# Optimization experiments

Measured on AMD Instinct MI355X. Metric: run time of the kernel, lower is better.

Reference implementation:

```python
import jax, jax.numpy as jnp
import numpy as np

N_NODES = 50000
N_EDGES = 600000  # incidence entries; hyperedge ids also live in [0, N_NODES)
HID = 128


def _prelu(x, a):
    return jnp.where(x >= 0, x, a * x)


def _hypergraph_conv(x, W, b, node_idx, edge_idx, num_nodes, num_hedges):
    # PyG HypergraphConv (use_attention=False, heads=1):
    # out = D^{-1} H B^{-1} H^T (X Theta) + bias
    xw = x @ W  # [N, F]
    ones = jnp.ones(node_idx.shape[0], dtype=x.dtype)
    D = jax.ops.segment_sum(ones, node_idx, num_segments=num_nodes)   # node degree
    B = jax.ops.segment_sum(ones, edge_idx, num_segments=num_hedges)  # hyperedge degree
    Dinv = jnp.where(D > 0, 1.0 / D, 0.0)
    Binv = jnp.where(B > 0, 1.0 / B, 0.0)
    # node -> hyperedge aggregation, scaled by B^{-1}
    m = jax.ops.segment_sum(xw[node_idx], edge_idx, num_segments=num_hedges) * Binv[:, None]
    # hyperedge -> node aggregation, scaled by D^{-1}
    out = jax.ops.segment_sum(m[edge_idx], node_idx, num_segments=num_nodes) * Dinv[:, None]
    return out + b


def setup_inputs() -> dict:
    key = jax.random.key(0)
    k1, k2, k3, k4, k5 = jax.random.split(key, 5)
    x = jax.random.normal(k1, (N_NODES, HID), dtype=jnp.float32)
    hyper_edge_index = jax.random.randint(k2, (2, N_EDGES), 0, N_NODES, dtype=jnp.int64)
    # kaiming-normal-ish linear weights, zero biases (per init_weights)
    std = float(np.sqrt(2.0 / HID))
    W1 = jax.random.normal(k3, (HID, HID), dtype=jnp.float32) * std
    W2 = jax.random.normal(k4, (HID, HID), dtype=jnp.float32) * std
    b1 = jnp.zeros((HID,), dtype=jnp.float32)
    b2 = jnp.zeros((HID,), dtype=jnp.float32)
    prelu_a = jnp.full((1,), 0.25, dtype=jnp.float32)  # nn.PReLU default
    return {"x": x, "hyper_edge_index": hyper_edge_index,
            "W1": W1, "b1": b1, "W2": W2, "b2": b2, "prelu_a": prelu_a}


def reference(x, hyper_edge_index, W1, b1, W2, b2, prelu_a):
    node_idx = hyper_edge_index[0]
    edge_idx = hyper_edge_index[1]
    h = _hypergraph_conv(x, W1, b1, node_idx, edge_idx, N_NODES, N_NODES)
    h = _prelu(h, prelu_a)
    h = _hypergraph_conv(h, W2, b2, node_idx, edge_idx, N_NODES, N_NODES)
    h = h + x  # residual
    return _prelu(h, prelu_a)
```

## Files before the change

kernel.cpp:

```cpp
#include <hip/hip_runtime.h>

typedef unsigned short u16;
typedef unsigned int   u32;
typedef unsigned long long u64;

#define HID 128
#define KPB 256
#define NBMAX 512
#define IPB 2048
#define CAP 6144

typedef __bf16 bf16x8 __attribute__((ext_vector_type(8)));
typedef float  f32x4  __attribute__((ext_vector_type(4)));
typedef u32    u32x4  __attribute__((ext_vector_type(4)));

__device__ inline float u2f(u32 u){ union{u32 u;float f;} v; v.u=u; return v.f; }
__device__ inline u32   f2u(float f){ union{float f;u32 u;} v; v.f=f; return v.u; }
__device__ inline u32  f2bfu(float f){ u32 b=f2u(f); return ((b + 0x7FFFu + ((b>>16)&1u))>>16)&0xFFFFu; }
__device__ inline float blo(u32 u){ return u2f(u<<16); }
__device__ inline float bhi(u32 u){ return u2f(u & 0xFFFF0000u); }
__device__ inline u32  pk(float lo, float hi){ return (f2bfu(hi)<<16) | f2bfu(lo); }


__global__ __launch_bounds__(256) void k_hist_wfrag(const int* __restrict__ nidx, const int* __restrict__ eidx,
                                                    int* __restrict__ hist, int nE, int nN, int nb, int nhb,
                                                    const float* __restrict__ W1, const float* __restrict__ W2,
                                                    u16* __restrict__ W1f, u16* __restrict__ W2f){
    __shared__ int h[NBMAX];
    if ((int)blockIdx.x < nhb){
        for (int t=threadIdx.x; t<nb; t+=256) h[t]=0;
        __syncthreads();
        int base = blockIdx.x*IPB;
        for (int k=threadIdx.x; k<IPB; k+=256){
            int j = base+k;
            if (j < nE){
                atomicAdd(&h[nidx[j]>>8], 1);
                atomicAdd(&h[(nN+eidx[j])>>8], 1);
            }
        }
        __syncthreads();
        for (int t=threadIdx.x; t<nb; t+=256) if (h[t]) atomicAdd(&hist[t], h[t]);
    } else {
        int gid = ((int)blockIdx.x - nhb)*256 + threadIdx.x;
        const float* W = (gid < 16384) ? W1 : W2;
        u16* Wf = (gid < 16384) ? W1f : W2f;
        int id = gid & 16383;
        int i = id & 7, l = (id>>3)&63, j = (id>>9)&7, s = id>>12;
        Wf[id] = (u16)f2bfu(W[(s*32 + ((l>>4)<<3) + i)*HID + (j<<4) + (l&15)]);
    }
}

__global__ __launch_bounds__(256) void k_part_gemm(const int* __restrict__ nidx, const int* __restrict__ eidx,
                                                   const int* __restrict__ hist, int* __restrict__ bfill,
                                                   u64* __restrict__ pairs, int nE, int nN, int nb, int npb,
                                                   const float* __restrict__ A, const u16* __restrict__ Wf,
                                                   u16* __restrict__ C, int M){
    __shared__ int h[NBMAX], rsv[NBMAX], fl[NBMAX], bb[NBMAX], sd[256];
    int t = threadIdx.x;
    if ((int)blockIdx.x < npb){
        for (int i=t; i<nb; i+=256){ h[i]=0; fl[i]=0; }
        __syncthreads();
        int base = blockIdx.x*IPB;
        for (int k=t; k<IPB; k+=256){
            int j = base+k;
            if (j < nE){
                atomicAdd(&h[nidx[j]>>8], 1);
                atomicAdd(&h[(nN+eidx[j])>>8], 1);
            }
        }
        int c0 = (2*t   < nb) ? hist[2*t]   : 0;
        int c1 = (2*t+1 < nb) ? hist[2*t+1] : 0;
        int s = c0 + c1;
        sd[t] = s; __syncthreads();
        for (int o=1;o<256;o<<=1){ int u = (t>=o)? sd[t-o] : 0; __syncthreads(); sd[t]+=u; __syncthreads(); }
        int ex = sd[t] - s;
        if (2*t   < nb) bb[2*t]   = ex;
        if (2*t+1 < nb) bb[2*t+1] = ex + c0;
        __syncthreads();
        for (int i=t; i<nb; i+=256){ if (h[i]) rsv[i] = bb[i] + atomicAdd(&bfill[i], h[i]); }
        __syncthreads();
        for (int k=t; k<IPB; k+=256){
            int j = base+k;
            if (j < nE){
                int n = nidx[j], e = eidx[j];
                int b1 = n>>8;
                int p1 = rsv[b1] + atomicAdd(&fl[b1], 1);
                pairs[p1] = ((u64)(u32)n << 32) | (u32)e;
                int k2 = nN + e;
                int b2 = k2>>8;
                int p2 = rsv[b2] + atomicAdd(&fl[b2], 1);
                pairs[p2] = ((u64)(u32)k2 << 32) | (u32)n;
            }
        }
    } else {
        int wave = ((int)blockIdx.x - npb)*4 + (t>>6);
        int lane = t & 63;
        int rtiles = M >> 4;
        if (wave >= rtiles) return;
        int row0 = wave << 4;
        const float* Arow = A + (size_t)(row0 + (lane&15))*HID + ((lane>>4)<<3);
        const bf16x8* Wp = reinterpret_cast<const bf16x8*>(Wf) + lane;
        f32x4 acc[8];
        #pragma unroll
        for (int j=0;j<8;++j) acc[j] = (f32x4){0.f,0.f,0.f,0.f};
        #pragma unroll
        for (int s=0;s<4;++s){
            float4 f0 = *reinterpret_cast<const float4*>(Arow + s*32);
            float4 f1 = *reinterpret_cast<const float4*>(Arow + s*32 + 4);
            union { u16 h[8]; bf16x8 v; } au;
            au.h[0]=(u16)f2bfu(f0.x); au.h[1]=(u16)f2bfu(f0.y); au.h[2]=(u16)f2bfu(f0.z); au.h[3]=(u16)f2bfu(f0.w);
            au.h[4]=(u16)f2bfu(f1.x); au.h[5]=(u16)f2bfu(f1.y); au.h[6]=(u16)f2bfu(f1.z); au.h[7]=(u16)f2bfu(f1.w);
            #pragma unroll
            for (int j=0;j<8;++j){
                bf16x8 b = Wp[(s*8 + j)*64];
                acc[j] = __builtin_amdgcn_mfma_f32_16x16x32_bf16(au.v, b, acc[j], 0, 0, 0);
            }
        }
        int r0 = row0 + ((lane>>4)<<2);
        int c0 = lane & 15;
        #pragma unroll
        for (int j=0;j<8;++j){
            size_t sb = ((size_t)(j>>2)*M)*64 + ((j&3)<<4) + c0;
            #pragma unroll
            for (int r=0;r<4;++r){
                __builtin_nontemporal_store((u16)f2bfu(acc[j][r]), &C[sb + (size_t)(r0+r)*64]);
            }
        }
    }
}

__global__ __launch_bounds__(256) void k_bucket(const u64* __restrict__ pairs, const int* __restrict__ hist,
                                                int* __restrict__ csr, int* __restrict__ off,
                                                int nkeys, int nb, int total){
    __shared__ int cntS[KPB];
    __shared__ int fillS[KPB];
    __shared__ int bbS[NBMAX+1];
    __shared__ int sd[256];
    __shared__ int vals[CAP];
    int b = blockIdx.x;
    int t = threadIdx.x;
    if (b == 0 && t == 0) off[nkeys] = total;
    int c0 = (2*t   < nb) ? hist[2*t]   : 0;
    int c1 = (2*t+1 < nb) ? hist[2*t+1] : 0;
    int s = c0 + c1;
    sd[t] = s; __syncthreads();
    for (int o=1;o<256;o<<=1){ int u = (t>=o)? sd[t-o] : 0; __syncthreads(); sd[t]+=u; __syncthreads(); }
    int ex = sd[t] - s;
    if (2*t   <= nb) bbS[2*t]   = ex;
    if (2*t+1 <= nb) bbS[2*t+1] = ex + c0;
    __syncthreads();
    int base = bbS[b];
    int n = bbS[b+1] - base;
    int k0 = b * KPB;

    cntS[t] = 0;
    __syncthreads();
    for (int i=t; i<n; i+=256){
        u64 p = pairs[base+i];
        atomicAdd(&cntS[(int)(p>>32) - k0], 1);
    }
    __syncthreads();
    int c = cntS[t];
    __syncthreads();
    fillS[t] = c; __syncthreads();
    for (int o=1;o<256;o<<=1){ int u = (t>=o)? fillS[t-o] : 0; __syncthreads(); fillS[t]+=u; __syncthreads(); }
    int ex2 = fillS[t] - c;
    __syncthreads();
    fillS[t] = ex2;
    __syncthreads();
    int k = k0 + t;
    if (k < nkeys) off[k] = base + ex2;
    bool fits = (n <= CAP);
    for (int i=t; i<n; i+=256){
        u64 p = pairs[base+i];
        int kl = (int)(p>>32) - k0;
        int pos = atomicAdd(&fillS[kl], 1);
        if (fits) vals[pos] = (int)(u32)p;
        else      csr[base+pos] = (int)(u32)p;
    }
    __syncthreads();
    if (fits){
        for (int i=t; i<n; i+=256) csr[base+i] = vals[i];
    }
}

template<int MODE>
__global__ __launch_bounds__(256) void k_aggs(const u32* __restrict__ tab, const int* __restrict__ csr,
                                              const int* __restrict__ off, void* __restrict__ outp,
                                              const float* __restrict__ bias, const float* __restrict__ resid,
                                              const float* __restrict__ aptr, int nrows){
    int slice = blockIdx.x & 1;
    int dt    = blockIdx.x >> 1;
    int t = threadIdx.x;
    int lane = t & 63;
    int grp = lane >> 3, c8 = lane & 7;
    int d = dt*32 + ((t>>6)<<3) + grp;
    if (d >= nrows) return;
    int start = off[d], end = off[d+1];
    int deg = end - start;
    const u32* tslice = tab + (size_t)slice*nrows*32 + (c8<<2);

    float a0=0.f,a1=0.f,a2=0.f,a3=0.f,a4=0.f,a5=0.f,a6=0.f,a7=0.f;
    int pos = start;
    for (; pos + 8 <= end; pos += 8){
        int j0 = csr[pos+0]; int j1 = csr[pos+1]; int j2 = csr[pos+2]; int j3 = csr[pos+3];
        int j4 = csr[pos+4]; int j5 = csr[pos+5]; int j6 = csr[pos+6]; int j7 = csr[pos+7];
        u32x4 v0 = *reinterpret_cast<const u32x4*>(tslice + (size_t)j0*32);
        u32x4 v1 = *reinterpret_cast<const u32x4*>(tslice + (size_t)j1*32);
        u32x4 v2 = *reinterpret_cast<const u32x4*>(tslice + (size_t)j2*32);
        u32x4 v3 = *reinterpret_cast<const u32x4*>(tslice + (size_t)j3*32);
        u32x4 v4 = *reinterpret_cast<const u32x4*>(tslice + (size_t)j4*32);
        u32x4 v5 = *reinterpret_cast<const u32x4*>(tslice + (size_t)j5*32);
        u32x4 v6 = *reinterpret_cast<const u32x4*>(tslice + (size_t)j6*32);
        u32x4 v7 = *reinterpret_cast<const u32x4*>(tslice + (size_t)j7*32);
        a0 += blo(v0.x)+blo(v1.x)+blo(v2.x)+blo(v3.x)+blo(v4.x)+blo(v5.x)+blo(v6.x)+blo(v7.x);
        a1 += bhi(v0.x)+bhi(v1.x)+bhi(v2.x)+bhi(v3.x)+bhi(v4.x)+bhi(v5.x)+bhi(v6.x)+bhi(v7.x);
        a2 += blo(v0.y)+blo(v1.y)+blo(v2.y)+blo(v3.y)+blo(v4.y)+blo(v5.y)+blo(v6.y)+blo(v7.y);
        a3 += bhi(v0.y)+bhi(v1.y)+bhi(v2.y)+bhi(v3.y)+bhi(v4.y)+bhi(v5.y)+bhi(v6.y)+bhi(v7.y);
        a4 += blo(v0.z)+blo(v1.z)+blo(v2.z)+blo(v3.z)+blo(v4.z)+blo(v5.z)+blo(v6.z)+blo(v7.z);
        a5 += bhi(v0.z)+bhi(v1.z)+bhi(v2.z)+bhi(v3.z)+bhi(v4.z)+bhi(v5.z)+bhi(v6.z)+bhi(v7.z);
        a6 += blo(v0.w)+blo(v1.w)+blo(v2.w)+blo(v3.w)+blo(v4.w)+blo(v5.w)+blo(v6.w)+blo(v7.w);
        a7 += bhi(v0.w)+bhi(v1.w)+bhi(v2.w)+bhi(v3.w)+bhi(v4.w)+bhi(v5.w)+bhi(v6.w)+bhi(v7.w);
    }
    for (; pos < end; pos += 4){
        int lim = end - pos;
        int j0 = csr[pos];
        int j1 = (lim > 1) ? csr[pos+1] : j0;
        int j2 = (lim > 2) ? csr[pos+2] : j0;
        int j3 = (lim > 3) ? csr[pos+3] : j0;
        u32x4 z = (u32x4){0u,0u,0u,0u};
        u32x4 v0 = *reinterpret_cast<const u32x4*>(tslice + (size_t)j0*32);
        u32x4 v1 = *reinterpret_cast<const u32x4*>(tslice + (size_t)j1*32);
        u32x4 v2 = *reinterpret_cast<const u32x4*>(tslice + (size_t)j2*32);
        u32x4 v3 = *reinterpret_cast<const u32x4*>(tslice + (size_t)j3*32);
        v1 = (lim > 1) ? v1 : z;
        v2 = (lim > 2) ? v2 : z;
        v3 = (lim > 3) ? v3 : z;
        a0 += blo(v0.x)+blo(v1.x)+blo(v2.x)+blo(v3.x);
        a1 += bhi(v0.x)+bhi(v1.x)+bhi(v2.x)+bhi(v3.x);
        a2 += blo(v0.y)+blo(v1.y)+blo(v2.y)+blo(v3.y);
        a3 += bhi(v0.y)+bhi(v1.y)+bhi(v2.y)+bhi(v3.y);
        a4 += blo(v0.z)+blo(v1.z)+blo(v2.z)+blo(v3.z);
        a5 += bhi(v0.z)+bhi(v1.z)+bhi(v2.z)+bhi(v3.z);
        a6 += blo(v0.w)+blo(v1.w)+blo(v2.w)+blo(v3.w);
        a7 += bhi(v0.w)+bhi(v1.w)+bhi(v2.w)+bhi(v3.w);
    }
    float s = (deg > 0) ? 1.0f/(float)deg : 0.f;
    a0*=s; a1*=s; a2*=s; a3*=s; a4*=s; a5*=s; a6*=s; a7*=s;
    if constexpr (MODE >= 1){
        const f32x4* bp = reinterpret_cast<const f32x4*>(bias + slice*64 + (c8<<3));
        f32x4 b0 = bp[0], b1v = bp[1];
        a0+=b0.x; a1+=b0.y; a2+=b0.z; a3+=b0.w;
        a4+=b1v.x; a5+=b1v.y; a6+=b1v.z; a7+=b1v.w;
        if constexpr (MODE == 2){
            const f32x4* rp = reinterpret_cast<const f32x4*>(resid + (size_t)d*HID + slice*64 + (c8<<3));
            f32x4 r0 = rp[0], r1 = rp[1];
            a0+=r0.x; a1+=r0.y; a2+=r0.z; a3+=r0.w;
            a4+=r1.x; a5+=r1.y; a6+=r1.z; a7+=r1.w;
        }
        float al = aptr[0];
        a0 = (a0>=0.f)? a0 : al*a0;  a1 = (a1>=0.f)? a1 : al*a1;
        a2 = (a2>=0.f)? a2 : al*a2;  a3 = (a3>=0.f)? a3 : al*a3;
        a4 = (a4>=0.f)? a4 : al*a4;  a5 = (a5>=0.f)? a5 : al*a5;
        a6 = (a6>=0.f)? a6 : al*a6;  a7 = (a7>=0.f)? a7 : al*a7;
    }
    if constexpr (MODE == 2){
        f32x4* op = reinterpret_cast<f32x4*>((float*)outp + (size_t)d*HID + slice*64 + (c8<<3));
        __builtin_nontemporal_store((f32x4){a0,a1,a2,a3}, op);
        __builtin_nontemporal_store((f32x4){a4,a5,a6,a7}, op + 1);
    } else if constexpr (MODE == 1){
        u32x4 wv4 = (u32x4){ pk(a0,a1), pk(a2,a3), pk(a4,a5), pk(a6,a7) };
        __builtin_nontemporal_store(wv4,
            reinterpret_cast<u32x4*>((u32*)outp + (size_t)d*64 + slice*32 + (c8<<2)));
    } else {
        u32x4 wv4 = (u32x4){ pk(a0,a1), pk(a2,a3), pk(a4,a5), pk(a6,a7) };
        __builtin_nontemporal_store(wv4,
            reinterpret_cast<u32x4*>((u32*)outp + ((size_t)slice*nrows + d)*32 + (c8<<2)));
    }
}

__global__ __launch_bounds__(256) void k_gemm_bf(const u16* __restrict__ A, const u16* __restrict__ Wf,
                                                 u16* __restrict__ C, int M){
    int wave = blockIdx.x*4 + ((int)threadIdx.x>>6);
    int lane = threadIdx.x & 63;
    int rtiles = M >> 4;
    if (wave >= rtiles) return;
    int row0 = wave << 4;
    const u16* Arow = A + (size_t)(row0 + (lane&15))*HID + ((lane>>4)<<3);
    const bf16x8* Wp = reinterpret_cast<const bf16x8*>(Wf) + lane;
    f32x4 acc[8];
    #pragma unroll
    for (int j=0;j<8;++j) acc[j] = (f32x4){0.f,0.f,0.f,0.f};
    #pragma unroll
    for (int s=0;s<4;++s){
        bf16x8 a = *reinterpret_cast<const bf16x8*>(Arow + s*32);
        #pragma unroll
        for (int j=0;j<8;++j){
            bf16x8 b = Wp[(s*8 + j)*64];
            acc[j] = __builtin_amdgcn_mfma_f32_16x16x32_bf16(a, b, acc[j], 0, 0, 0);
        }
    }
    int r0 = row0 + ((lane>>4)<<2);
    int c0 = lane & 15;
    #pragma unroll
    for (int j=0;j<8;++j){
        size_t sb = ((size_t)(j>>2)*M)*64 + ((j&3)<<4) + c0;
        #pragma unroll
        for (int r=0;r<4;++r){
            __builtin_nontemporal_store((u16)f2bfu(acc[j][r]), &C[sb + (size_t)(r0+r)*64]);
        }
    }
}

extern "C" void kernel_launch(void* const* d_in, const int* in_sizes, int n_in,
                              void* d_out, int out_size, void* d_ws, size_t ws_size,
                              hipStream_t stream){
    (void)n_in; (void)out_size; (void)ws_size;
    const float* x  = (const float*)d_in[0];
    const int*  hei = (const int*)  d_in[1];
    const float* W1 = (const float*)d_in[2];
    const float* b1 = (const float*)d_in[3];
    const float* W2 = (const float*)d_in[4];
    const float* b2 = (const float*)d_in[5];
    const float* ap = (const float*)d_in[6];

    const int nN = in_sizes[0] / HID;
    const int nE = in_sizes[1] / 2;
    const int* nidx = hei;
    const int* eidx = hei + nE;
    const int nkeys = 2*nN;
    const int nb    = (nkeys + KPB - 1) / KPB;

    char* w = (char*)d_ws;
    size_t o = 0;
    auto alloc = [&](size_t bytes)->void*{
        void* p = (void*)(w + o);
        o += (bytes + 255) & ~(size_t)255;
        return p;
    };
    int* hist  = (int*)alloc((size_t)NBMAX*sizeof(int));
    int* bfill = (int*)alloc((size_t)NBMAX*sizeof(int));
    int* off   = (int*)alloc(((size_t)nkeys+1)*sizeof(int));
    int* csr   = (int*)alloc((size_t)2*nE*sizeof(int));
    u64* pairs = (u64*)alloc((size_t)2*nE*sizeof(u64));
    u16* bufB  = (u16*)alloc((size_t)nN*HID*sizeof(u16));
    u16* bufC  = (u16*)alloc((size_t)nN*HID*sizeof(u16));
    u16* bufH  = (u16*)alloc((size_t)nN*HID*sizeof(u16));
    u16* w1f   = (u16*)alloc((size_t)HID*HID*sizeof(u16));
    u16* w2f   = (u16*)alloc((size_t)HID*HID*sizeof(u16));

    hipMemsetAsync(hist, 0, (size_t)2*NBMAX*sizeof(int), stream);

    const int pgrid  = (nE + IPB - 1)/IPB;
    const int rtiles = nN/16;
    const int ggrid  = (rtiles + 3)/4;
    const int dblk   = (nN + 31)/32;
    const int agrid  = 2*dblk;

    k_hist_wfrag<<<pgrid + 128, 256, 0, stream>>>(nidx, eidx, hist, nE, nN, nb, pgrid, W1, W2, w1f, w2f);
    k_part_gemm<<<pgrid + ggrid, 256, 0, stream>>>(nidx, eidx, hist, bfill, pairs, nE, nN, nb, pgrid,
                                                   x, w1f, bufB, nN);
    k_bucket<<<nb, 256, 0, stream>>>(pairs, hist, csr, off, nkeys, nb, 2*nE);

    k_aggs<0><<<agrid, 256, 0, stream>>>((const u32*)bufB, csr, off + nN, bufC, nullptr, nullptr, nullptr, nN);
    k_aggs<1><<<agrid, 256, 0, stream>>>((const u32*)bufC, csr, off, bufH, b1, nullptr, ap, nN);
    k_gemm_bf<<<ggrid, 256, 0, stream>>>(bufH, w2f, bufB, nN);
    k_aggs<0><<<agrid, 256, 0, stream>>>((const u32*)bufB, csr, off + nN, bufC, nullptr, nullptr, nullptr, nN);
    k_aggs<2><<<agrid, 256, 0, stream>>>((const u32*)bufC, csr, off, d_out, b2, x, ap, nN);
}
```

Before: 228.7 us.

## Assign one wavefront per row in gather aggregation with cross-group shuffle reduction

The gather-aggregation kernel now gives each 64-lane wavefront a single destination row instead of eight rows. The row's neighbour indices are loaded coalesced into lanes and broadcast with shuffles. The eight 8-lane groups each gather a different neighbour, then a butterfly shuffle reduction combines their partial sums. This targets load imbalance from uneven row degrees within a wave and adds memory-level parallelism per row. In exchange the grid is eight times larger, the kernel pays extra shuffle-reduction work, and the index load can read up to 63 entries past the end of a row.

```diff
diff --git a/kernel.cpp b/kernel.cpp
--- a/kernel.cpp
+++ b/kernel.cpp
@@ -193,58 +193,38 @@
     int dt    = blockIdx.x >> 1;
     int t = threadIdx.x;
     int lane = t & 63;
-    int grp = lane >> 3, c8 = lane & 7;
-    int d = dt*32 + ((t>>6)<<3) + grp;
+    int d = dt*4 + (t>>6);
     if (d >= nrows) return;
     int start = off[d], end = off[d+1];
     int deg = end - start;
+    int g  = lane >> 3, c8 = lane & 7;
     const u32* tslice = tab + (size_t)slice*nrows*32 + (c8<<2);
 
     float a0=0.f,a1=0.f,a2=0.f,a3=0.f,a4=0.f,a5=0.f,a6=0.f,a7=0.f;
-    int pos = start;
-    for (; pos + 8 <= end; pos += 8){
-        int j0 = csr[pos+0]; int j1 = csr[pos+1]; int j2 = csr[pos+2]; int j3 = csr[pos+3];
-        int j4 = csr[pos+4]; int j5 = csr[pos+5]; int j6 = csr[pos+6]; int j7 = csr[pos+7];
-        u32x4 v0 = *reinterpret_cast<const u32x4*>(tslice + (size_t)j0*32);
-        u32x4 v1 = *reinterpret_cast<const u32x4*>(tslice + (size_t)j1*32);
-        u32x4 v2 = *reinterpret_cast<const u32x4*>(tslice + (size_t)j2*32);
-        u32x4 v3 = *reinterpret_cast<const u32x4*>(tslice + (size_t)j3*32);
-        u32x4 v4 = *reinterpret_cast<const u32x4*>(tslice + (size_t)j4*32);
-        u32x4 v5 = *reinterpret_cast<const u32x4*>(tslice + (size_t)j5*32);
-        u32x4 v6 = *reinterpret_cast<const u32x4*>(tslice + (size_t)j6*32);
-        u32x4 v7 = *reinterpret_cast<const u32x4*>(tslice + (size_t)j7*32);
-        a0 += blo(v0.x)+blo(v1.x)+blo(v2.x)+blo(v3.x)+blo(v4.x)+blo(v5.x)+blo(v6.x)+blo(v7.x);
-        a1 += bhi(v0.x)+bhi(v1.x)+bhi(v2.x)+bhi(v3.x)+bhi(v4.x)+bhi(v5.x)+bhi(v6.x)+bhi(v7.x);
-        a2 += blo(v0.y)+blo(v1.y)+blo(v2.y)+blo(v3.y)+blo(v4.y)+blo(v5.y)+blo(v6.y)+blo(v7.y);
-        a3 += bhi(v0.y)+bhi(v1.y)+bhi(v2.y)+bhi(v3.y)+bhi(v4.y)+bhi(v5.y)+bhi(v6.y)+bhi(v7.y);
-        a4 += blo(v0.z)+blo(v1.z)+blo(v2.z)+blo(v3.z)+blo(v4.z)+blo(v5.z)+blo(v6.z)+blo(v7.z);
-        a5 += bhi(v0.z)+bhi(v1.z)+bhi(v2.z)+bhi(v3.z)+bhi(v4.z)+bhi(v5.z)+bhi(v6.z)+bhi(v7.z);
-        a6 += blo(v0.w)+blo(v1.w)+blo(v2.w)+blo(v3.w)+blo(v4.w)+blo(v5.w)+blo(v6.w)+blo(v7.w);
-        a7 += bhi(v0.w)+bhi(v1.w)+bhi(v2.w)+bhi(v3.w)+bhi(v4.w)+bhi(v5.w)+bhi(v6.w)+bhi(v7.w);
-    }
-    for (; pos < end; pos += 4){
-        int lim = end - pos;
-        int j0 = csr[pos];
-        int j1 = (lim > 1) ? csr[pos+1] : j0;
-        int j2 = (lim > 2) ? csr[pos+2] : j0;
-        int j3 = (lim > 3) ? csr[pos+3] : j0;
-        u32x4 z = (u32x4){0u,0u,0u,0u};
-        u32x4 v0 = *reinterpret_cast<const u32x4*>(tslice + (size_t)j0*32);
-        u32x4 v1 = *reinterpret_cast<const u32x4*>(tslice + (size_t)j1*32);
-        u32x4 v2 = *reinterpret_cast<const u32x4*>(tslice + (size_t)j2*32);
-        u32x4 v3 = *reinterpret_cast<const u32x4*>(tslice + (size_t)j3*32);
-        v1 = (lim > 1) ? v1 : z;
-        v2 = (lim > 2) ? v2 : z;
-        v3 = (lim > 3) ? v3 : z;
-        a0 += blo(v0.x)+blo(v1.x)+blo(v2.x)+blo(v3.x);
-        a1 += bhi(v0.x)+bhi(v1.x)+bhi(v2.x)+bhi(v3.x);
-        a2 += blo(v0.y)+blo(v1.y)+blo(v2.y)+blo(v3.y);
-        a3 += bhi(v0.y)+bhi(v1.y)+bhi(v2.y)+bhi(v3.y);
-        a4 += blo(v0.z)+blo(v1.z)+blo(v2.z)+blo(v3.z);
-        a5 += bhi(v0.z)+bhi(v1.z)+bhi(v2.z)+bhi(v3.z);
-        a6 += blo(v0.w)+blo(v1.w)+blo(v2.w)+blo(v3.w);
-        a7 += bhi(v0.w)+bhi(v1.w)+bhi(v2.w)+bhi(v3.w);
-    }
+    for (int w = start; w < end; w += 64){
+        int widx = csr[w + lane];
+        int nit = end - w; if (nit > 64) nit = 64;
+        int iters = (nit + 7) >> 3;
+        for (int it = 0; it < iters; ++it){
+            int sl  = (it<<3) + g;
+            int slc = (sl < nit) ? sl : (nit-1);
+            int idx = __shfl(widx, slc, 64);
+            u32x4 v = *reinterpret_cast<const u32x4*>(tslice + (size_t)idx*32);
+            if (sl >= nit) v = (u32x4){0u,0u,0u,0u};
+            a0 += blo(v.x); a1 += bhi(v.x);
+            a2 += blo(v.y); a3 += bhi(v.y);
+            a4 += blo(v.z); a5 += bhi(v.z);
+            a6 += blo(v.w); a7 += bhi(v.w);
+        }
+    }
+    #pragma unroll
+    for (int m = 8; m < 64; m <<= 1){
+        a0 += __shfl_xor(a0, m, 64); a1 += __shfl_xor(a1, m, 64);
+        a2 += __shfl_xor(a2, m, 64); a3 += __shfl_xor(a3, m, 64);
+        a4 += __shfl_xor(a4, m, 64); a5 += __shfl_xor(a5, m, 64);
+        a6 += __shfl_xor(a6, m, 64); a7 += __shfl_xor(a7, m, 64);
+    }
+    if (g != 0) return;
     float s = (deg > 0) ? 1.0f/(float)deg : 0.f;
     a0*=s; a1*=s; a2*=s; a3*=s; a4*=s; a5*=s; a6*=s; a7*=s;
     if constexpr (MODE >= 1){
@@ -354,7 +334,7 @@
     const int pgrid  = (nE + IPB - 1)/IPB;
     const int rtiles = nN/16;
     const int ggrid  = (rtiles + 3)/4;
-    const int dblk   = (nN + 31)/32;
+    const int dblk   = (nN + 3)/4;
     const int agrid  = 2*dblk;
 
     k_hist_wfrag<<<pgrid + 128, 256, 0, stream>>>(nidx, eidx, hist, nE, nN, nb, pgrid, W1, W2, w1f, w2f);
```

Result: slower. 303.1 us (+32.5%).
